# Kernel tuning notes

Measured on AMD Instinct MI355X. Metric: run time of the kernel, lower is better.

Reference implementation:

```python
import jax, jax.numpy as jnp
import numpy as np

N = 20000      # nodes
E = 320000     # edges
D = 128        # h feature dim
L = 2          # EGCL layers
MH = 256       # mlp_m hidden
MO = 128       # mlp_m output (message dim)
XH = 256       # mlp_x hidden
HH = 256       # mlp_h hidden
MIN = 2 * D + 1  # 257: cat(h_i, h_j, ||dx||^2)


def silu(z):
    return z * jax.nn.sigmoid(z)


def setup_inputs() -> dict:
    key = jax.random.key(0)
    ks = jax.random.split(key, 18)
    s = 0.05
    return {
        "edge_index": jax.random.randint(ks[0], (2, E), 0, N, dtype=jnp.int64 if jax.config.jax_enable_x64 else jnp.int32),
        "h": jax.random.normal(ks[1], (N, D), dtype=jnp.float32),
        "x": jax.random.normal(ks[2], (N, 3), dtype=jnp.float32),
        # per-layer stacked MLP params
        "Wm1": jax.random.normal(ks[3], (L, MIN, MH), dtype=jnp.float32) * s,
        "bm1": jnp.zeros((L, MH), dtype=jnp.float32),
        "Wm2": jax.random.normal(ks[4], (L, MH, MO), dtype=jnp.float32) * s,
        "bm2": jnp.zeros((L, MO), dtype=jnp.float32),
        "Wx1": jax.random.normal(ks[5], (L, MIN, XH), dtype=jnp.float32) * s,
        "bx1": jnp.zeros((L, XH), dtype=jnp.float32),
        "Wx2": jax.random.normal(ks[6], (L, XH, 3), dtype=jnp.float32) * s,
        "bx2": jnp.zeros((L, 3), dtype=jnp.float32),
        "Wh1": jax.random.normal(ks[7], (L, D + MO, HH), dtype=jnp.float32) * s,
        "bh1": jnp.zeros((L, HH), dtype=jnp.float32),
        "Wh2": jax.random.normal(ks[8], (L, HH, D), dtype=jnp.float32) * s,
        "bh2": jnp.zeros((L, D), dtype=jnp.float32),
        "Wa": jax.random.normal(ks[9], (L, MO, 1), dtype=jnp.float32) * s,
        "ba": jnp.zeros((L, 1), dtype=jnp.float32),
    }


def reference(edge_index, h, x, Wm1, bm1, Wm2, bm2, Wx1, bx1, Wx2, bx2,
              Wh1, bh1, Wh2, bh2, Wa, ba):
    # flow='target_to_source': i = edge_index[0], j = edge_index[1],
    # aggregation (scatter-sum) indexed by edge_index[0].
    src = edge_index[0]
    dst = edge_index[1]
    n_nodes = h.shape[0]
    n_layers = Wm1.shape[0]
    for l in range(n_layers):
        hi, hj = h[src], h[dst]                       # [E, D] gathers
        diff = x[src] - x[dst]                        # [E, 3]
        d2 = jnp.sum(diff * diff, axis=1, keepdims=True)  # ||dx||^2, [E, 1]
        feat = jnp.concatenate([hi, hj, d2], axis=1)  # [E, 2D+1]
        # --- h message: mlp_m + sigmoid attention gate ---
        m = silu(feat @ Wm1[l] + bm1[l]) @ Wm2[l] + bm2[l]   # [E, MO]
        m = m * jax.nn.sigmoid(m @ Wa[l] + ba[l])
        agg_h = jax.ops.segment_sum(m, src, num_segments=n_nodes)  # [N, MO]
        new_h = silu(jnp.concatenate([h, agg_h], axis=1) @ Wh1[l] + bh1[l]) @ Wh2[l] + bh2[l]
        # --- x message (uses OLD h, as in original forward) ---
        mx = silu(feat @ Wx1[l] + bx1[l]) @ Wx2[l] + bx2[l]  # [E, 3]
        # NOTE: original uses torch.norm(coords_i - coords_j) with NO dim ->
        # a single global Frobenius norm over all edges; reproduced faithfully.
        gnorm = jnp.sqrt(jnp.sum(diff * diff))
        xm = diff * mx / (gnorm + 1.0)                # [E, 3]
        new_x = x + jax.ops.segment_sum(xm, src, num_segments=n_nodes)
        h, x = new_h, new_x
    return (h, x)
```

## Files before the change

kernel.cpp:

```cpp
#include <hip/hip_runtime.h>
#include <hip/hip_bf16.h>

#define N_NODES 20000
#define N_EDGES 320000
#define D 128

typedef __attribute__((ext_vector_type(8))) short short8;
typedef __attribute__((ext_vector_type(4))) float f32x4;

__device__ __forceinline__ float sigmoid_f(float z) { return 1.f / (1.f + __expf(-z)); }
__device__ __forceinline__ float silu_f(float z) { return z * sigmoid_f(z); }
__device__ __forceinline__ short f2bf(float f) {
    union { float f; unsigned u; } a; a.f = f;
    unsigned r = a.u + 0x7fff + ((a.u >> 16) & 1);
    return (short)(r >> 16);
}
__device__ __forceinline__ float bf2f(short s) {
    union { unsigned u; float f; } a; a.u = ((unsigned)(unsigned short)s) << 16;
    return a.f;
}

__global__ void hist_kernel(const int* __restrict__ ei, int* __restrict__ hist) {
    int e = blockIdx.x * 256 + threadIdx.x;
    if (e < N_EDGES) atomicAdd(&hist[ei[e]], 1);
}

__global__ void scan_kernel(const int* __restrict__ hist, int* __restrict__ offs) {
    __shared__ int part[1024];
    __shared__ int ppre[1024];
    int t = threadIdx.x;
    int base = t * 20;
    int s = 0;
    for (int j = 0; j < 20; j++) { int i = base + j; if (i < N_NODES) s += hist[i]; }
    part[t] = s;
    __syncthreads();
    if (t == 0) { int acc = 0; for (int i = 0; i < 1024; i++) { ppre[i] = acc; acc += part[i]; } }
    __syncthreads();
    int run = ppre[t];
    for (int j = 0; j < 20; j++) {
        int i = base + j;
        if (i < N_NODES) { offs[i] = run; run += hist[i]; }
    }
}

__global__ void scatter_kernel(const int* __restrict__ ei, const int* __restrict__ offs,
                               int* __restrict__ cursor,
                               int* __restrict__ es, int* __restrict__ ed) {
    int e = blockIdx.x * 256 + threadIdx.x;
    if (e < N_EDGES) {
        int s = ei[e], d = ei[N_EDGES + e];
        int p = offs[s] + atomicAdd(&cursor[s], 1);
        es[p] = s; ed[p] = d;
    }
}

__global__ void precompute_kernel(const int* __restrict__ es, const int* __restrict__ ed,
                                  const float* __restrict__ x,
                                  float* __restrict__ gsum) {
    int e = blockIdx.x * blockDim.x + threadIdx.x;
    float local = 0.f;
    if (e < N_EDGES) {
        int s = es[e];
        int d = ed[e];
        float dx = x[s * 3 + 0] - x[d * 3 + 0];
        float dy = x[s * 3 + 1] - x[d * 3 + 1];
        float dz = x[s * 3 + 2] - x[d * 3 + 2];
        local = dx * dx + dy * dy + dz * dz;
    }
    #pragma unroll
    for (int o = 32; o > 0; o >>= 1) local += __shfl_down(local, o, 64);
    if ((threadIdx.x & 63) == 0) atomicAdd(gsum, local);
}

__global__ void prep_weights(const float* __restrict__ Wm1, const float* __restrict__ Wx1,
                             const float* __restrict__ Wm2, const float* __restrict__ Wh1,
                             const float* __restrict__ Wh2, const float* __restrict__ Wx2,
                             short* __restrict__ WcatT, short* __restrict__ Wm2T,
                             short* __restrict__ Wh1T, short* __restrict__ Wh2T,
                             short* __restrict__ Wx2T) {
    int idx = blockIdx.x * 256 + threadIdx.x;
    if (idx < 131072) {
        int seg = idx >> 15, r = idx & 32767, k = r >> 8, c = r & 255;
        const float* s = (seg == 0) ? Wm1 : (seg == 1) ? Wx1
                        : (seg == 2) ? Wm1 + 128 * 256 : Wx1 + 128 * 256;
        WcatT[(size_t)(seg * 256 + c) * 128 + k] = f2bf(s[k * 256 + c]);
    } else if (idx < 163840) {
        int r = idx - 131072, k = r >> 7, c = r & 127;
        Wm2T[c * 256 + k] = f2bf(Wm2[k * 128 + c]);
    } else if (idx < 229376) {
        int r = idx - 163840, k = r >> 8, c = r & 255;
        Wh1T[c * 256 + k] = f2bf(Wh1[k * 256 + c]);
    } else if (idx < 262144) {
        int r = idx - 229376, k = r >> 7, c = r & 127;
        Wh2T[c * 256 + k] = f2bf(Wh2[k * 128 + c]);
    } else {
        int r = idx - 262144, c = r >> 8, k = r & 255;
        Wx2T[c * 256 + k] = (c < 3) ? f2bf(Wx2[k * 3 + c]) : (short)0;
    }
}

__global__ __launch_bounds__(256, 4) void tgemm_kernel(const float* __restrict__ h,
        const short* __restrict__ WcatT, short* __restrict__ T) {
    int tid = threadIdx.x, w = tid >> 6, l = tid & 63;
    int l15 = l & 15, kg = l >> 4;
    int rowbase = blockIdx.x * 64 + w * 16;
    int cg = blockIdx.y;
    int arow = rowbase + l15; if (arow >= N_NODES) arow = N_NODES - 1;
    f32x4 acc[16];
    #pragma unroll
    for (int ct = 0; ct < 16; ct++) acc[ct] = (f32x4){0.f, 0.f, 0.f, 0.f};
    #pragma unroll
    for (int ks = 0; ks < 4; ks++) {
        int kb = ks * 32 + kg * 8;
        const f32x4* hp = (const f32x4*)(h + (size_t)arow * 128 + kb);
        f32x4 h0 = hp[0], h1 = hp[1];
        short8 a;
        a[0] = f2bf(h0.x); a[1] = f2bf(h0.y); a[2] = f2bf(h0.z); a[3] = f2bf(h0.w);
        a[4] = f2bf(h1.x); a[5] = f2bf(h1.y); a[6] = f2bf(h1.z); a[7] = f2bf(h1.w);
        #pragma unroll
        for (int ct = 0; ct < 16; ct++) {
            short8 b = *(const short8*)(WcatT + (size_t)(cg * 256 + ct * 16 + l15) * 128 + kb);
            acc[ct] = __builtin_amdgcn_mfma_f32_16x16x32_bf16(a, b, acc[ct], 0, 0, 0);
        }
    }
    #pragma unroll
    for (int ct = 0; ct < 16; ct++) {
        #pragma unroll
        for (int r = 0; r < 4; r++) {
            int node = rowbase + kg * 4 + r;
            if (node < N_NODES)
                T[(size_t)node * 1024 + cg * 256 + ct * 16 + l15] = f2bf(acc[ct][r]);
        }
    }
}

__global__ __launch_bounds__(256, 6) void edge_kernel(
    const int* __restrict__ es, const int* __restrict__ ed,
    const short* __restrict__ T, const float* __restrict__ xc,
    const float* __restrict__ gsum,
    const float* __restrict__ Wm1r, const float* __restrict__ bm1,
    const short* __restrict__ Wm2T, const float* __restrict__ bm2,
    const float* __restrict__ Wa, const float* __restrict__ ba,
    const float* __restrict__ Wx1r, const float* __restrict__ bx1,
    const short* __restrict__ Wx2T, const float* __restrict__ bx2,
    float* __restrict__ agg_h, float* __restrict__ aggx) {
    __shared__ float sdiff[64][4];
    int tid = threadIdx.x, w = tid >> 6, l = tid & 63;
    int l15 = l & 15, kg = l >> 4;
    int ebase = blockIdx.x * 64 + w * 16;
    int e = ebase + l15;
    int src = es[e], dst = ed[e];
    float dfx = xc[src * 3 + 0] - xc[dst * 3 + 0];
    float dfy = xc[src * 3 + 1] - xc[dst * 3 + 1];
    float dfz = xc[src * 3 + 2] - xc[dst * 3 + 2];
    float d2v = dfx * dfx + dfy * dfy + dfz * dfz;
    if (kg == 0) {
        sdiff[w * 16 + l15][0] = dfx;
        sdiff[w * 16 + l15][1] = dfy;
        sdiff[w * 16 + l15][2] = dfz;
    }
    __syncthreads();

    int srow[4];
    #pragma unroll
    for (int r = 0; r < 4; r++) srow[r] = es[ebase + kg * 4 + r];

    f32x4 acc[8];
    #pragma unroll
    for (int ct = 0; ct < 8; ct++) { float bv = bm2[ct * 16 + l15]; acc[ct] = (f32x4){bv, bv, bv, bv}; }
    #pragma unroll
    for (int ks = 0; ks < 8; ks++) {
        int cb = ks * 32 + kg * 8;
        short8 ts = *(const short8*)(T + (size_t)src * 1024 + cb);
        short8 td = *(const short8*)(T + (size_t)dst * 1024 + 512 + cb);
        f32x4 w0 = ((const f32x4*)(Wm1r + cb))[0], w1 = ((const f32x4*)(Wm1r + cb))[1];
        f32x4 b0 = ((const f32x4*)(bm1 + cb))[0], b1 = ((const f32x4*)(bm1 + cb))[1];
        float wv[8], bv[8];
        *(f32x4*)&wv[0] = w0; *(f32x4*)&wv[4] = w1;
        *(f32x4*)&bv[0] = b0; *(f32x4*)&bv[4] = b1;
        short8 a;
        #pragma unroll
        for (int i = 0; i < 8; i++) {
            float z = bf2f(ts[i]) + bf2f(td[i]) + d2v * wv[i] + bv[i];
            a[i] = f2bf(silu_f(z));
        }
        #pragma unroll
        for (int ct = 0; ct < 8; ct++) {
            short8 b = *(const short8*)(Wm2T + (size_t)(ct * 16 + l15) * 256 + cb);
            acc[ct] = __builtin_amdgcn_mfma_f32_16x16x32_bf16(a, b, acc[ct], 0, 0, 0);
        }
    }
    float part[4] = {0.f, 0.f, 0.f, 0.f};
    #pragma unroll
    for (int ct = 0; ct < 8; ct++) {
        float wa = Wa[ct * 16 + l15];
        #pragma unroll
        for (int r = 0; r < 4; r++) part[r] += acc[ct][r] * wa;
    }
    #pragma unroll
    for (int m = 1; m < 16; m <<= 1) {
        #pragma unroll
        for (int r = 0; r < 4; r++) part[r] += __shfl_xor(part[r], m, 64);
    }
    float ba0 = ba[0];
    float gate[4];
    #pragma unroll
    for (int r = 0; r < 4; r++) gate[r] = sigmoid_f(part[r] + ba0);
    #pragma unroll
    for (int ct = 0; ct < 8; ct++) {
        int c = ct * 16 + l15;
        float run = acc[ct][0] * gate[0];
        #pragma unroll
        for (int r = 1; r < 4; r++) {
            float v = acc[ct][r] * gate[r];
            if (srow[r] == srow[r - 1]) {
                run += v;
            } else {
                atomicAdd(&agg_h[(size_t)srow[r - 1] * 128 + c], run);
                run = v;
            }
        }
        atomicAdd(&agg_h[(size_t)srow[3] * 128 + c], run);
    }

    float bxi = (l15 < 3) ? bx2[l15] : 0.f;
    f32x4 accx = (f32x4){bxi, bxi, bxi, bxi};
    #pragma unroll
    for (int ks = 0; ks < 8; ks++) {
        int cb = ks * 32 + kg * 8;
        short8 ts = *(const short8*)(T + (size_t)src * 1024 + 256 + cb);
        short8 td = *(const short8*)(T + (size_t)dst * 1024 + 768 + cb);
        f32x4 w0 = ((const f32x4*)(Wx1r + cb))[0], w1 = ((const f32x4*)(Wx1r + cb))[1];
        f32x4 b0 = ((const f32x4*)(bx1 + cb))[0], b1 = ((const f32x4*)(bx1 + cb))[1];
        float wv[8], bv[8];
        *(f32x4*)&wv[0] = w0; *(f32x4*)&wv[4] = w1;
        *(f32x4*)&bv[0] = b0; *(f32x4*)&bv[4] = b1;
        short8 a;
        #pragma unroll
        for (int i = 0; i < 8; i++) {
            float z = bf2f(ts[i]) + bf2f(td[i]) + d2v * wv[i] + bv[i];
            a[i] = f2bf(silu_f(z));
        }
        short8 b = *(const short8*)(Wx2T + (size_t)l15 * 256 + cb);
        accx = __builtin_amdgcn_mfma_f32_16x16x32_bf16(a, b, accx, 0, 0, 0);
    }
    if (l15 < 3) {
        float gn = sqrtf(gsum[0]);
        float invg = 1.f / (gn + 1.f);
        #pragma unroll
        for (int r = 0; r < 4; r++) {
            float df = sdiff[w * 16 + kg * 4 + r][l15];
            atomicAdd(&aggx[(size_t)srow[r] * 3 + l15], df * accx[r] * invg);
        }
    }
}

__global__ __launch_bounds__(256, 4) void node_kernel(
    const float* __restrict__ hc, const float* __restrict__ xc,
    const float* __restrict__ agg_h, const float* __restrict__ aggx,
    const short* __restrict__ Wh1T, const float* __restrict__ bh1,
    const short* __restrict__ Wh2T, const float* __restrict__ bh2,
    float* __restrict__ ho, float* __restrict__ xo) {
    __shared__ short sH[64][264];
    int tid = threadIdx.x, w = tid >> 6, l = tid & 63;
    int l15 = l & 15, kg = l >> 4;
    int nbase = blockIdx.x * 64;
    int arow = nbase + w * 16 + l15;
    int arc = (arow < N_NODES) ? arow : (N_NODES - 1);

    f32x4 acc1[16];
    #pragma unroll
    for (int ct = 0; ct < 16; ct++) { float bv = bh1[ct * 16 + l15]; acc1[ct] = (f32x4){bv, bv, bv, bv}; }
    #pragma unroll
    for (int ks = 0; ks < 8; ks++) {
        int kb = ks * 32 + kg * 8;
        const float* sp = (kb < 128) ? (hc + (size_t)arc * 128 + kb)
                                     : (agg_h + (size_t)arc * 128 + (kb - 128));
        f32x4 h0 = ((const f32x4*)sp)[0], h1 = ((const f32x4*)sp)[1];
        short8 a;
        a[0] = f2bf(h0.x); a[1] = f2bf(h0.y); a[2] = f2bf(h0.z); a[3] = f2bf(h0.w);
        a[4] = f2bf(h1.x); a[5] = f2bf(h1.y); a[6] = f2bf(h1.z); a[7] = f2bf(h1.w);
        #pragma unroll
        for (int ct = 0; ct < 16; ct++) {
            short8 b = *(const short8*)(Wh1T + (size_t)(ct * 16 + l15) * 256 + kb);
            acc1[ct] = __builtin_amdgcn_mfma_f32_16x16x32_bf16(a, b, acc1[ct], 0, 0, 0);
        }
    }
    #pragma unroll
    for (int ct = 0; ct < 16; ct++)
        #pragma unroll
        for (int r = 0; r < 4; r++)
            sH[w * 16 + kg * 4 + r][ct * 16 + l15] = f2bf(silu_f(acc1[ct][r]));
    __syncthreads();

    f32x4 acc2[8];
    #pragma unroll
    for (int ct = 0; ct < 8; ct++) { float bv = bh2[ct * 16 + l15]; acc2[ct] = (f32x4){bv, bv, bv, bv}; }
    #pragma unroll
    for (int ks = 0; ks < 8; ks++) {
        int kb = ks * 32 + kg * 8;
        short8 a = *(const short8*)&sH[w * 16 + l15][kb];
        #pragma unroll
        for (int ct = 0; ct < 8; ct++) {
            short8 b = *(const short8*)(Wh2T + (size_t)(ct * 16 + l15) * 256 + kb);
            acc2[ct] = __builtin_amdgcn_mfma_f32_16x16x32_bf16(a, b, acc2[ct], 0, 0, 0);
        }
    }
    #pragma unroll
    for (int ct = 0; ct < 8; ct++)
        #pragma unroll
        for (int r = 0; r < 4; r++) {
            int node = nbase + w * 16 + kg * 4 + r;
            if (node < N_NODES) ho[(size_t)node * 128 + ct * 16 + l15] = acc2[ct][r];
        }

    if (tid < 192) {
        int nn = tid / 3, c = tid - nn * 3;
        int node = nbase + nn;
        if (node < N_NODES)
            xo[(size_t)node * 3 + c] = xc[(size_t)node * 3 + c] + aggx[(size_t)node * 3 + c];
    }
}

extern "C" void kernel_launch(void* const* d_in, const int* in_sizes, int n_in,
                              void* d_out, int out_size, void* d_ws, size_t ws_size,
                              hipStream_t stream) {
    const int* ei = (const int*)d_in[0];
    const float* h_in = (const float*)d_in[1];
    const float* x_in = (const float*)d_in[2];
    const float* Wm1 = (const float*)d_in[3];
    const float* bm1 = (const float*)d_in[4];
    const float* Wm2 = (const float*)d_in[5];
    const float* bm2 = (const float*)d_in[6];
    const float* Wx1 = (const float*)d_in[7];
    const float* bx1 = (const float*)d_in[8];
    const float* Wx2 = (const float*)d_in[9];
    const float* bx2 = (const float*)d_in[10];
    const float* Wh1 = (const float*)d_in[11];
    const float* bh1 = (const float*)d_in[12];
    const float* Wh2 = (const float*)d_in[13];
    const float* bh2 = (const float*)d_in[14];
    const float* Wa = (const float*)d_in[15];
    const float* ba = (const float*)d_in[16];

    char* wsb = (char*)d_ws;
    short* T      = (short*)wsb;  wsb += (size_t)N_NODES * 1024 * 2;
    short* WcatT  = (short*)wsb;  wsb += (size_t)1024 * 128 * 2;
    short* Wm2T   = (short*)wsb;  wsb += (size_t)128 * 256 * 2;
    short* Wh1T   = (short*)wsb;  wsb += (size_t)256 * 256 * 2;
    short* Wh2T   = (short*)wsb;  wsb += (size_t)128 * 256 * 2;
    short* Wx2T   = (short*)wsb;  wsb += (size_t)16 * 256 * 2;
    float* agg_h  = (float*)wsb;  wsb += (size_t)N_NODES * 128 * 4;
    float* aggx   = (float*)wsb;  wsb += (size_t)N_NODES * 3 * 4;
    int*   es     = (int*)wsb;    wsb += (size_t)N_EDGES * 4;
    int*   ed     = (int*)wsb;    wsb += (size_t)N_EDGES * 4;
    int*   hist   = (int*)wsb;    wsb += (size_t)N_NODES * 4;
    int*   cursor = (int*)wsb;    wsb += (size_t)N_NODES * 4;
    float* gsum   = (float*)wsb;  wsb += 16;
    int*   offs   = (int*)wsb;    wsb += (size_t)(N_NODES + 16) * 4;

    float* h_out_f = (float*)d_out;
    float* x_out_f = h_out_f + (size_t)N_NODES * D;

    hipMemsetAsync(hist, 0, sizeof(int) * N_NODES, stream);
    hipMemsetAsync(cursor, 0, sizeof(int) * N_NODES, stream);
    hist_kernel<<<(N_EDGES + 255) / 256, 256, 0, stream>>>(ei, hist);
    scan_kernel<<<1, 1024, 0, stream>>>(hist, offs);
    scatter_kernel<<<(N_EDGES + 255) / 256, 256, 0, stream>>>(ei, offs, cursor, es, ed);

    for (int l = 0; l < 2; l++) {
        const float* hc = (l == 0) ? h_in : h_out_f;
        const float* xc = (l == 0) ? x_in : x_out_f;
        float* ho = h_out_f;
        float* xo = x_out_f;

        const float* Wm1_l = Wm1 + (size_t)l * 257 * 256;
        const float* Wx1_l = Wx1 + (size_t)l * 257 * 256;

        hipMemsetAsync(gsum, 0, sizeof(float), stream);
        hipMemsetAsync(agg_h, 0, sizeof(float) * (size_t)N_NODES * 128, stream);
        hipMemsetAsync(aggx, 0, sizeof(float) * (size_t)N_NODES * 3, stream);

        prep_weights<<<1040, 256, 0, stream>>>(
            Wm1_l, Wx1_l, Wm2 + (size_t)l * 256 * 128,
            Wh1 + (size_t)l * 256 * 256, Wh2 + (size_t)l * 256 * 128,
            Wx2 + (size_t)l * 256 * 3,
            WcatT, Wm2T, Wh1T, Wh2T, Wx2T);

        precompute_kernel<<<(N_EDGES + 255) / 256, 256, 0, stream>>>(es, ed, xc, gsum);

        tgemm_kernel<<<dim3((N_NODES + 63) / 64, 4), 256, 0, stream>>>(hc, WcatT, T);

        edge_kernel<<<N_EDGES / 64, 256, 0, stream>>>(
            es, ed, T, xc, gsum,
            Wm1_l + 256 * 256, bm1 + (size_t)l * 256,
            Wm2T, bm2 + (size_t)l * 128,
            Wa + (size_t)l * 128, ba + l,
            Wx1_l + 256 * 256, bx1 + (size_t)l * 256,
            Wx2T, bx2 + (size_t)l * 3,
            agg_h, aggx);

        node_kernel<<<(N_NODES + 63) / 64, 256, 0, stream>>>(
            hc, xc, agg_h, aggx,
            Wh1T, bh1 + (size_t)l * 256,
            Wh2T, bh2 + (size_t)l * 128,
            ho, xo);
    }
}
```

Baseline: 1.155 ms.

## Split activations into bf16 hi/lo pairs, hoist weight prep, use a shuffle scan

Activations feeding the MFMA GEMMs (tgemm, edge mlp_m first layer, node Wh1) are split into bf16 high and low parts, and each is multiplied separately, doubling MFMA count to recover accuracy. Weight conversion for both layers moves to one launch before the loop, per-layer memsets are merged into one, the scan kernel uses wavefront shuffles instead of a serial loop, and the edge kernel drops its shared-memory diff buffer and __syncthreads in favour of shuffles. The accuracy fix adds compute and register pressure, while the other pieces cut launches and sync overhead.

```diff
diff --git a/kernel.cpp b/kernel.cpp
--- a/kernel.cpp
+++ b/kernel.cpp
@@ -19,6 +19,10 @@
     union { unsigned u; float f; } a; a.u = ((unsigned)(unsigned short)s) << 16;
     return a.f;
 }
+__device__ __forceinline__ void splitbf(float v, short &hi, short &lo) {
+    hi = f2bf(v);
+    lo = f2bf(v - bf2f(hi));
+}
 
 __global__ void hist_kernel(const int* __restrict__ ei, int* __restrict__ hist) {
     int e = blockIdx.x * 256 + threadIdx.x;
@@ -26,20 +30,32 @@
 }
 
 __global__ void scan_kernel(const int* __restrict__ hist, int* __restrict__ offs) {
-    __shared__ int part[1024];
-    __shared__ int ppre[1024];
+    __shared__ int wsum[16];
     int t = threadIdx.x;
     int base = t * 20;
+    int loc[20];
     int s = 0;
-    for (int j = 0; j < 20; j++) { int i = base + j; if (i < N_NODES) s += hist[i]; }
-    part[t] = s;
-    __syncthreads();
-    if (t == 0) { int acc = 0; for (int i = 0; i < 1024; i++) { ppre[i] = acc; acc += part[i]; } }
-    __syncthreads();
-    int run = ppre[t];
+    #pragma unroll
     for (int j = 0; j < 20; j++) {
         int i = base + j;
-        if (i < N_NODES) { offs[i] = run; run += hist[i]; }
+        int v = (i < N_NODES) ? hist[i] : 0;
+        loc[j] = s; s += v;
+    }
+    int lane = t & 63, wv = t >> 6;
+    int pref = s;
+    #pragma unroll
+    for (int o = 1; o < 64; o <<= 1) {
+        int y = __shfl_up(pref, o, 64);
+        if (lane >= o) pref += y;
+    }
+    if (lane == 63) wsum[wv] = pref;
+    __syncthreads();
+    if (t == 0) { int a = 0; for (int i = 0; i < 16; i++) { int v = wsum[i]; wsum[i] = a; a += v; } }
+    __syncthreads();
+    int tpref = pref - s + wsum[wv];
+    for (int j = 0; j < 20; j++) {
+        int i = base + j;
+        if (i < N_NODES) offs[i] = tpref + loc[j];
     }
 }
 
@@ -72,13 +88,26 @@
     if ((threadIdx.x & 63) == 0) atomicAdd(gsum, local);
 }
 
-__global__ void prep_weights(const float* __restrict__ Wm1, const float* __restrict__ Wx1,
-                             const float* __restrict__ Wm2, const float* __restrict__ Wh1,
-                             const float* __restrict__ Wh2, const float* __restrict__ Wx2,
-                             short* __restrict__ WcatT, short* __restrict__ Wm2T,
-                             short* __restrict__ Wh1T, short* __restrict__ Wh2T,
-                             short* __restrict__ Wx2T) {
-    int idx = blockIdx.x * 256 + threadIdx.x;
+__global__ void prep_weights(const float* __restrict__ Wm1g, const float* __restrict__ Wx1g,
+                             const float* __restrict__ Wm2g, const float* __restrict__ Wh1g,
+                             const float* __restrict__ Wh2g, const float* __restrict__ Wx2g,
+                             short* __restrict__ WcatTg, short* __restrict__ Wm2Tg,
+                             short* __restrict__ Wh1Tg, short* __restrict__ Wh2Tg,
+                             short* __restrict__ Wx2Tg) {
+    int b = blockIdx.x;
+    int l = (b >= 1040) ? 1 : 0; b -= l * 1040;
+    int idx = b * 256 + threadIdx.x;
+    const float* Wm1 = Wm1g + (size_t)l * 257 * 256;
+    const float* Wx1 = Wx1g + (size_t)l * 257 * 256;
+    const float* Wm2 = Wm2g + (size_t)l * 256 * 128;
+    const float* Wh1 = Wh1g + (size_t)l * 256 * 256;
+    const float* Wh2 = Wh2g + (size_t)l * 256 * 128;
+    const float* Wx2 = Wx2g + (size_t)l * 256 * 3;
+    short* WcatT = WcatTg + (size_t)l * 1024 * 128;
+    short* Wm2T  = Wm2Tg  + (size_t)l * 128 * 256;
+    short* Wh1T  = Wh1Tg  + (size_t)l * 256 * 256;
+    short* Wh2T  = Wh2Tg  + (size_t)l * 128 * 256;
+    short* Wx2T  = Wx2Tg  + (size_t)l * 16 * 256;
     if (idx < 131072) {
         int seg = idx >> 15, r = idx & 32767, k = r >> 8, c = r & 255;
         const float* s = (seg == 0) ? Wm1 : (seg == 1) ? Wx1
@@ -114,13 +143,16 @@
         int kb = ks * 32 + kg * 8;
         const f32x4* hp = (const f32x4*)(h + (size_t)arow * 128 + kb);
         f32x4 h0 = hp[0], h1 = hp[1];
-        short8 a;
-        a[0] = f2bf(h0.x); a[1] = f2bf(h0.y); a[2] = f2bf(h0.z); a[3] = f2bf(h0.w);
-        a[4] = f2bf(h1.x); a[5] = f2bf(h1.y); a[6] = f2bf(h1.z); a[7] = f2bf(h1.w);
+        float hv[8];
+        *(f32x4*)&hv[0] = h0; *(f32x4*)&hv[4] = h1;
+        short8 a_hi, a_lo;
+        #pragma unroll
+        for (int i = 0; i < 8; i++) { short hi, lo; splitbf(hv[i], hi, lo); a_hi[i] = hi; a_lo[i] = lo; }
         #pragma unroll
         for (int ct = 0; ct < 16; ct++) {
             short8 b = *(const short8*)(WcatT + (size_t)(cg * 256 + ct * 16 + l15) * 128 + kb);
-            acc[ct] = __builtin_amdgcn_mfma_f32_16x16x32_bf16(a, b, acc[ct], 0, 0, 0);
+            acc[ct] = __builtin_amdgcn_mfma_f32_16x16x32_bf16(a_lo, b, acc[ct], 0, 0, 0);
+            acc[ct] = __builtin_amdgcn_mfma_f32_16x16x32_bf16(a_hi, b, acc[ct], 0, 0, 0);
         }
     }
     #pragma unroll
@@ -144,7 +176,6 @@
     const float* __restrict__ Wx1r, const float* __restrict__ bx1,
     const short* __restrict__ Wx2T, const float* __restrict__ bx2,
     float* __restrict__ agg_h, float* __restrict__ aggx) {
-    __shared__ float sdiff[64][4];
     int tid = threadIdx.x, w = tid >> 6, l = tid & 63;
     int l15 = l & 15, kg = l >> 4;
     int ebase = blockIdx.x * 64 + w * 16;
@@ -154,12 +185,6 @@
     float dfy = xc[src * 3 + 1] - xc[dst * 3 + 1];
     float dfz = xc[src * 3 + 2] - xc[dst * 3 + 2];
     float d2v = dfx * dfx + dfy * dfy + dfz * dfz;
-    if (kg == 0) {
-        sdiff[w * 16 + l15][0] = dfx;
-        sdiff[w * 16 + l15][1] = dfy;
-        sdiff[w * 16 + l15][2] = dfz;
-    }
-    __syncthreads();
 
     int srow[4];
     #pragma unroll
@@ -178,16 +203,18 @@
         float wv[8], bv[8];
         *(f32x4*)&wv[0] = w0; *(f32x4*)&wv[4] = w1;
         *(f32x4*)&bv[0] = b0; *(f32x4*)&bv[4] = b1;
-        short8 a;
+        short8 a_hi, a_lo;
         #pragma unroll
         for (int i = 0; i < 8; i++) {
             float z = bf2f(ts[i]) + bf2f(td[i]) + d2v * wv[i] + bv[i];
-            a[i] = f2bf(silu_f(z));
+            short hi, lo; splitbf(silu_f(z), hi, lo);
+            a_hi[i] = hi; a_lo[i] = lo;
         }
         #pragma unroll
         for (int ct = 0; ct < 8; ct++) {
             short8 b = *(const short8*)(Wm2T + (size_t)(ct * 16 + l15) * 256 + cb);
-            acc[ct] = __builtin_amdgcn_mfma_f32_16x16x32_bf16(a, b, acc[ct], 0, 0, 0);
+            acc[ct] = __builtin_amdgcn_mfma_f32_16x16x32_bf16(a_lo, b, acc[ct], 0, 0, 0);
+            acc[ct] = __builtin_amdgcn_mfma_f32_16x16x32_bf16(a_hi, b, acc[ct], 0, 0, 0);
         }
     }
     float part[4] = {0.f, 0.f, 0.f, 0.f};
@@ -249,7 +276,10 @@
         float invg = 1.f / (gn + 1.f);
         #pragma unroll
         for (int r = 0; r < 4; r++) {
-            float df = sdiff[w * 16 + kg * 4 + r][l15];
+            int lsrc = kg * 4 + r;
+            float df = (l15 == 0) ? __shfl(dfx, lsrc, 64)
+                     : (l15 == 1) ? __shfl(dfy, lsrc, 64)
+                                  : __shfl(dfz, lsrc, 64);
             atomicAdd(&aggx[(size_t)srow[r] * 3 + l15], df * accx[r] * invg);
         }
     }
@@ -277,13 +307,16 @@
         const float* sp = (kb < 128) ? (hc + (size_t)arc * 128 + kb)
                                      : (agg_h + (size_t)arc * 128 + (kb - 128));
         f32x4 h0 = ((const f32x4*)sp)[0], h1 = ((const f32x4*)sp)[1];
-        short8 a;
-        a[0] = f2bf(h0.x); a[1] = f2bf(h0.y); a[2] = f2bf(h0.z); a[3] = f2bf(h0.w);
-        a[4] = f2bf(h1.x); a[5] = f2bf(h1.y); a[6] = f2bf(h1.z); a[7] = f2bf(h1.w);
+        float hv[8];
+        *(f32x4*)&hv[0] = h0; *(f32x4*)&hv[4] = h1;
+        short8 a_hi, a_lo;
+        #pragma unroll
+        for (int i = 0; i < 8; i++) { short hi, lo; splitbf(hv[i], hi, lo); a_hi[i] = hi; a_lo[i] = lo; }
         #pragma unroll
         for (int ct = 0; ct < 16; ct++) {
             short8 b = *(const short8*)(Wh1T + (size_t)(ct * 16 + l15) * 256 + kb);
-            acc1[ct] = __builtin_amdgcn_mfma_f32_16x16x32_bf16(a, b, acc1[ct], 0, 0, 0);
+            acc1[ct] = __builtin_amdgcn_mfma_f32_16x16x32_bf16(a_lo, b, acc1[ct], 0, 0, 0);
+            acc1[ct] = __builtin_amdgcn_mfma_f32_16x16x32_bf16(a_hi, b, acc1[ct], 0, 0, 0);
         }
     }
     #pragma unroll
@@ -345,28 +378,29 @@
 
     char* wsb = (char*)d_ws;
     short* T      = (short*)wsb;  wsb += (size_t)N_NODES * 1024 * 2;
-    short* WcatT  = (short*)wsb;  wsb += (size_t)1024 * 128 * 2;
-    short* Wm2T   = (short*)wsb;  wsb += (size_t)128 * 256 * 2;
-    short* Wh1T   = (short*)wsb;  wsb += (size_t)256 * 256 * 2;
-    short* Wh2T   = (short*)wsb;  wsb += (size_t)128 * 256 * 2;
-    short* Wx2T   = (short*)wsb;  wsb += (size_t)16 * 256 * 2;
+    short* WcatT  = (short*)wsb;  wsb += (size_t)2 * 1024 * 128 * 2;
+    short* Wm2T   = (short*)wsb;  wsb += (size_t)2 * 128 * 256 * 2;
+    short* Wh1T   = (short*)wsb;  wsb += (size_t)2 * 256 * 256 * 2;
+    short* Wh2T   = (short*)wsb;  wsb += (size_t)2 * 128 * 256 * 2;
+    short* Wx2T   = (short*)wsb;  wsb += (size_t)2 * 16 * 256 * 2;
     float* agg_h  = (float*)wsb;  wsb += (size_t)N_NODES * 128 * 4;
     float* aggx   = (float*)wsb;  wsb += (size_t)N_NODES * 3 * 4;
+    float* gsum   = (float*)wsb;  wsb += 16;
     int*   es     = (int*)wsb;    wsb += (size_t)N_EDGES * 4;
     int*   ed     = (int*)wsb;    wsb += (size_t)N_EDGES * 4;
     int*   hist   = (int*)wsb;    wsb += (size_t)N_NODES * 4;
     int*   cursor = (int*)wsb;    wsb += (size_t)N_NODES * 4;
-    float* gsum   = (float*)wsb;  wsb += 16;
     int*   offs   = (int*)wsb;    wsb += (size_t)(N_NODES + 16) * 4;
 
     float* h_out_f = (float*)d_out;
     float* x_out_f = h_out_f + (size_t)N_NODES * D;
 
-    hipMemsetAsync(hist, 0, sizeof(int) * N_NODES, stream);
-    hipMemsetAsync(cursor, 0, sizeof(int) * N_NODES, stream);
+    hipMemsetAsync(hist, 0, sizeof(int) * N_NODES * 2, stream);
     hist_kernel<<<(N_EDGES + 255) / 256, 256, 0, stream>>>(ei, hist);
     scan_kernel<<<1, 1024, 0, stream>>>(hist, offs);
     scatter_kernel<<<(N_EDGES + 255) / 256, 256, 0, stream>>>(ei, offs, cursor, es, ed);
+    prep_weights<<<2080, 256, 0, stream>>>(Wm1, Wx1, Wm2, Wh1, Wh2, Wx2,
+                                           WcatT, Wm2T, Wh1T, Wh2T, Wx2T);
 
     for (int l = 0; l < 2; l++) {
         const float* hc = (l == 0) ? h_in : h_out_f;
@@ -374,36 +408,28 @@
         float* ho = h_out_f;
         float* xo = x_out_f;
 
-        const float* Wm1_l = Wm1 + (size_t)l * 257 * 256;
-        const float* Wx1_l = Wx1 + (size_t)l * 257 * 256;
-
-        hipMemsetAsync(gsum, 0, sizeof(float), stream);
-        hipMemsetAsync(agg_h, 0, sizeof(float) * (size_t)N_NODES * 128, stream);
-        hipMemsetAsync(aggx, 0, sizeof(float) * (size_t)N_NODES * 3, stream);
-
-        prep_weights<<<1040, 256, 0, stream>>>(
-            Wm1_l, Wx1_l, Wm2 + (size_t)l * 256 * 128,
-            Wh1 + (size_t)l * 256 * 256, Wh2 + (size_t)l * 256 * 128,
-            Wx2 + (size_t)l * 256 * 3,
-            WcatT, Wm2T, Wh1T, Wh2T, Wx2T);
+        hipMemsetAsync(agg_h, 0,
+                       sizeof(float) * ((size_t)N_NODES * 128 + (size_t)N_NODES * 3) + 16,
+                       stream);
 
         precompute_kernel<<<(N_EDGES + 255) / 256, 256, 0, stream>>>(es, ed, xc, gsum);
 
-        tgemm_kernel<<<dim3((N_NODES + 63) / 64, 4), 256, 0, stream>>>(hc, WcatT, T);
+        tgemm_kernel<<<dim3((N_NODES + 63) / 64, 4), 256, 0, stream>>>(
+            hc, WcatT + (size_t)l * 1024 * 128, T);
 
         edge_kernel<<<N_EDGES / 64, 256, 0, stream>>>(
             es, ed, T, xc, gsum,
-            Wm1_l + 256 * 256, bm1 + (size_t)l * 256,
-            Wm2T, bm2 + (size_t)l * 128,
+            Wm1 + (size_t)l * 257 * 256 + 256 * 256, bm1 + (size_t)l * 256,
+            Wm2T + (size_t)l * 128 * 256, bm2 + (size_t)l * 128,
             Wa + (size_t)l * 128, ba + l,
-            Wx1_l + 256 * 256, bx1 + (size_t)l * 256,
-            Wx2T, bx2 + (size_t)l * 3,
+            Wx1 + (size_t)l * 257 * 256 + 256 * 256, bx1 + (size_t)l * 256,
+            Wx2T + (size_t)l * 16 * 256, bx2 + (size_t)l * 3,
             agg_h, aggx);
 
         node_kernel<<<(N_NODES + 63) / 64, 256, 0, stream>>>(
             hc, xc, agg_h, aggx,
-            Wh1T, bh1 + (size_t)l * 256,
-            Wh2T, bh2 + (size_t)l * 128,
+            Wh1T + (size_t)l * 256 * 256, bh1 + (size_t)l * 256,
+            Wh2T + (size_t)l * 128 * 256, bh2 + (size_t)l * 128,
             ho, xo);
     }
 }
```

Result: slower. 1.237 ms (+7.1%).
